# Optimization experiments

Hardware: AMD Instinct MI355X
Metric: run time of the kernel (lower is better)

The kernel has to match this reference:

```python
import jax, jax.numpy as jnp
import numpy as np

C_MID = 32  # inChannels // 8
# Packing order matches torch loop: diagonal offset -i for i in 0..C-1,
# i.e. pairs (j+i, j) for j in 0..C-1-i, concatenated.
_ROWS = np.concatenate([np.arange(C_MID - i) + i for i in range(C_MID)])
_COLS = np.concatenate([np.arange(C_MID - i) for i in range(C_MID)])


def _bn_relu(y, g, b, m, v, eps=1e-5):
    # y: (B, C, H, W); per-channel affine BN (eval-style) + relu
    inv = g / jnp.sqrt(v + eps)
    return jax.nn.relu(y * inv[:, None, None] + (b - m * inv)[:, None, None])


def setup_inputs() -> dict:
    key = jax.random.key(0)
    ks = jax.random.split(key, 14)
    B, Cin, H, W = 16, 256, 64, 64
    mid, T, Cout = C_MID, C_MID * (C_MID + 1) // 2, 256
    return {
        "x": jax.random.normal(ks[0], (B, Cin, H, W), jnp.float32),
        "w1": jax.random.normal(ks[1], (mid, Cin), jnp.float32) * 0.05,
        "b1": jax.random.normal(ks[2], (mid,), jnp.float32) * 0.05,
        "g1": jax.random.uniform(ks[3], (mid,), jnp.float32, 0.5, 1.5),
        "be1": jax.random.normal(ks[4], (mid,), jnp.float32) * 0.1,
        "m1": jax.random.normal(ks[5], (mid,), jnp.float32) * 0.1,
        "v1": jax.random.uniform(ks[6], (mid,), jnp.float32, 0.5, 1.5),
        "w2": jax.random.normal(ks[7], (Cout, T), jnp.float32) * 0.05,
        "b2": jax.random.normal(ks[8], (Cout,), jnp.float32) * 0.05,
        "g2": jax.random.uniform(ks[9], (Cout,), jnp.float32, 0.5, 1.5),
        "be2": jax.random.normal(ks[10], (Cout,), jnp.float32) * 0.1,
        "m2": jax.random.normal(ks[11], (Cout,), jnp.float32) * 0.1,
        "v2": jax.random.uniform(ks[12], (Cout,), jnp.float32, 0.5, 1.5),
    }


def reference(x, w1, b1, g1, be1, m1, v1, w2, b2, g2, be2, m2, v2):
    # dimReduceLayer1: 1x1 conv + BN + relu
    y = jnp.einsum('bchw,oc->bohw', x, w1) + b1[:, None, None]
    y = _bn_relu(y, g1, be1, m1, v1)                       # (B, mid, H, W)
    yb = jnp.transpose(y, (0, 2, 3, 1))                    # (B, H, W, mid)
    rows = jnp.asarray(_ROWS)
    cols = jnp.asarray(_COLS)
    # Packed lower-triangular bilinear features, exactly the torch diagonal+cat order.
    packed = yb[..., rows] * yb[..., cols]                 # (B, H, W, T)
    # dimReduceLayer2: 1x1 conv + BN + relu
    z = jnp.einsum('bhwt,ot->bohw', packed, w2) + b2[:, None, None]
    return _bn_relu(z, g2, be2, m2, v2)
```

## Files before the change

### kernel.cpp

```cpp
#include <hip/hip_runtime.h>

#define EPS 1e-5f

typedef float f32x4 __attribute__((ext_vector_type(4)));
typedef short bf16x8 __attribute__((ext_vector_type(8)));

__device__ __forceinline__ unsigned short f2bf(float f) {
  unsigned int u = __builtin_bit_cast(unsigned int, f);
  u = (u + 0x7FFFu + ((u >> 16) & 1u)) >> 16;
  return (unsigned short)u;
}

__global__ __launch_bounds__(256) void k_prep(
    const float* __restrict__ w1, const float* __restrict__ b1,
    const float* __restrict__ g1, const float* __restrict__ be1,
    const float* __restrict__ m1, const float* __restrict__ v1,
    const float* __restrict__ w2, const float* __restrict__ b2,
    const float* __restrict__ g2, const float* __restrict__ be2,
    const float* __restrict__ m2, const float* __restrict__ v2,
    float* __restrict__ beta1, float* __restrict__ beta2,
    unsigned short* __restrict__ w1b, unsigned short* __restrict__ w2f)
{
  int t = blockIdx.x * 256 + threadIdx.x;
  if (t < 139264) {
    int j = t & 7, l = (t >> 3) & 63, g = t >> 9;
    int ct = g & 15, ks = g >> 4;
    int k = ks * 32 + (l >> 4) * 8 + j;
    int ch = ct * 16 + (l & 15);
    float val = 0.f;
    if (k < 528) {
      float s2 = g2[ch] * rsqrtf(v2[ch] + EPS);
      val = w2[ch * 528 + k] * s2;
    }
    w2f[t] = f2bf(val);
  }
  if (t < 8192) {
    int j = t & 7, l = (t >> 3) & 63, g = t >> 9;
    int ct = g & 1, ks = g >> 1;
    int c = ks * 32 + (l >> 4) * 8 + j;
    int m = ct * 16 + (l & 15);
    float s1 = g1[m] * rsqrtf(v1[m] + EPS);
    w1b[t] = f2bf(w1[m * 256 + c] * s1);
  }
  if (t < 32) {
    float s1 = g1[t] * rsqrtf(v1[t] + EPS);
    beta1[t] = (b1[t] - m1[t]) * s1 + be1[t];
  }
  if (t < 256) {
    float s2 = g2[t] * rsqrtf(v2[t] + EPS);
    beta2[t] = (b2[t] - m2[t]) * s2 + be2[t];
  }
}

__global__ __launch_bounds__(256) void k_fused(
    const float* __restrict__ x, const unsigned short* __restrict__ w1b,
    const float* __restrict__ beta1, const unsigned short* __restrict__ w2f,
    const float* __restrict__ beta2, float* __restrict__ out)
{
  __shared__ __align__(16) unsigned short pk[64 * 548];
  __shared__ float yf[64 * 33];
  int tid = threadIdx.x;
  int wv = tid >> 6, lane = tid & 63;
  int l15 = lane & 15, l4 = lane >> 4;
  int pb = blockIdx.x * 64;
  int b = pb >> 12, hw0 = pb & 4095;
  const float* xb = x + ((size_t)b << 20) + hw0;

  unsigned short* xt = pk;
  {
    int q = tid & 15;
    int c40 = tid >> 4;
    for (int pass = 0; pass < 4; ++pass) {
      int c4 = c40 + pass * 16;
      float4 v[4];
#pragma unroll
      for (int i = 0; i < 4; ++i)
        v[i] = *(const float4*)&xb[(size_t)(4 * c4 + i) * 4096 + 4 * q];
#pragma unroll
      for (int s = 0; s < 4; ++s) {
        float e0 = ((const float*)&v[0])[s];
        float e1 = ((const float*)&v[1])[s];
        float e2 = ((const float*)&v[2])[s];
        float e3 = ((const float*)&v[3])[s];
        unsigned int lo = (unsigned int)f2bf(e0) | ((unsigned int)f2bf(e1) << 16);
        unsigned int hi = (unsigned int)f2bf(e2) | ((unsigned int)f2bf(e3) << 16);
        *(uint2*)&xt[(4 * q + s) * 276 + 4 * c4] = make_uint2(lo, hi);
      }
    }
  }
  __syncthreads();

  {
    f32x4 acc1[2];
    acc1[0] = (f32x4){0.f, 0.f, 0.f, 0.f};
    acc1[1] = (f32x4){0.f, 0.f, 0.f, 0.f};
    const uint4* w1b4 = (const uint4*)w1b;
    int px = wv * 16 + l15;
    for (int ks = 0; ks < 8; ++ks) {
      union { uint4 q; bf16x8 v; } A0, A1, B;
      A0.q = w1b4[(ks * 2 + 0) * 64 + lane];
      A1.q = w1b4[(ks * 2 + 1) * 64 + lane];
      const unsigned short* s = &xt[px * 276 + ks * 32 + l4 * 8];
      uint2 lo = *(const uint2*)s;
      uint2 hi = *(const uint2*)(s + 4);
      B.q = make_uint4(lo.x, lo.y, hi.x, hi.y);
      acc1[0] = __builtin_amdgcn_mfma_f32_16x16x32_bf16(A0.v, B.v, acc1[0], 0, 0, 0);
      acc1[1] = __builtin_amdgcn_mfma_f32_16x16x32_bf16(A1.v, B.v, acc1[1], 0, 0, 0);
    }
    __syncthreads();
#pragma unroll
    for (int ct = 0; ct < 2; ++ct) {
      int m0 = ct * 16 + l4 * 4;
#pragma unroll
      for (int r = 0; r < 4; ++r) {
        float yv = fmaxf(acc1[ct][r] + beta1[m0 + r], 0.f);
        yf[px * 33 + m0 + r] = yv;
      }
    }
  }
  __syncthreads();

  {
    int p2 = tid & 63, set = tid >> 6;
    const float* yr = &yf[p2 * 33];
    unsigned short* pr = &pk[p2 * 548];
    for (int i = set; i < 32; i += 4) {
      int base = 32 * i - (i * (i - 1)) / 2;
      int len = 32 - i;
      int j = 0;
      if (base & 1) {
        pr[base] = f2bf(yr[i] * yr[0]);
        j = 1;
      }
      for (; j + 1 < len; j += 2) {
        float a = yr[i + j] * yr[j];
        float c = yr[i + j + 1] * yr[j + 1];
        *(unsigned int*)&pr[base + j] =
            (unsigned int)f2bf(a) | ((unsigned int)f2bf(c) << 16);
      }
      if (j < len) pr[base + j] = f2bf(yr[i + j] * yr[j]);
    }
    if (tid < 64) {
      unsigned int* pru = (unsigned int*)pk + tid * 274;
#pragma unroll
      for (int z = 264; z < 274; ++z) pru[z] = 0u;
    }
  }
  __syncthreads();

  f32x4 acc[4][4];
#pragma unroll
  for (int a = 0; a < 4; ++a)
#pragma unroll
    for (int c = 0; c < 4; ++c)
      acc[a][c] = (f32x4){0.f, 0.f, 0.f, 0.f};

  const uint4* w2f4 = (const uint4*)w2f;
  for (int ks = 0; ks < 17; ++ks) {
    union { uint4 q; bf16x8 v; } A[4], B[4];
#pragma unroll
    for (int ctl = 0; ctl < 4; ++ctl)
      A[ctl].q = w2f4[(ks * 16 + wv * 4 + ctl) * 64 + lane];
#pragma unroll
    for (int pt = 0; pt < 4; ++pt) {
      const unsigned short* src = &pk[(pt * 16 + l15) * 548 + ks * 32 + l4 * 8];
      uint2 lo = *(const uint2*)src;
      uint2 hi = *(const uint2*)(src + 4);
      B[pt].q = make_uint4(lo.x, lo.y, hi.x, hi.y);
    }
#pragma unroll
    for (int pt = 0; pt < 4; ++pt)
#pragma unroll
      for (int ctl = 0; ctl < 4; ++ctl)
        acc[pt][ctl] = __builtin_amdgcn_mfma_f32_16x16x32_bf16(
            A[ctl].v, B[pt].v, acc[pt][ctl], 0, 0, 0);
  }

  float bet[4][4];
#pragma unroll
  for (int ctl = 0; ctl < 4; ++ctl)
#pragma unroll
    for (int r = 0; r < 4; ++r)
      bet[ctl][r] = beta2[(wv * 4 + ctl) * 16 + l4 * 4 + r];

#pragma unroll
  for (int pt = 0; pt < 4; ++pt) {
    int hw = hw0 + pt * 16 + l15;
#pragma unroll
    for (int ctl = 0; ctl < 4; ++ctl) {
      int ch = (wv * 4 + ctl) * 16 + l4 * 4;
#pragma unroll
      for (int r = 0; r < 4; ++r) {
        float v = fmaxf(acc[pt][ctl][r] + bet[ctl][r], 0.f);
        out[(((size_t)b * 256 + (ch + r)) << 12) + hw] = v;
      }
    }
  }
}

extern "C" void kernel_launch(void* const* d_in, const int* in_sizes, int n_in,
                              void* d_out, int out_size, void* d_ws, size_t ws_size,
                              hipStream_t stream)
{
  const float* x   = (const float*)d_in[0];
  const float* w1  = (const float*)d_in[1];
  const float* b1  = (const float*)d_in[2];
  const float* g1  = (const float*)d_in[3];
  const float* be1 = (const float*)d_in[4];
  const float* m1  = (const float*)d_in[5];
  const float* v1  = (const float*)d_in[6];
  const float* w2  = (const float*)d_in[7];
  const float* b2  = (const float*)d_in[8];
  const float* g2  = (const float*)d_in[9];
  const float* be2 = (const float*)d_in[10];
  const float* m2  = (const float*)d_in[11];
  const float* v2  = (const float*)d_in[12];

  char* ws = (char*)d_ws;
  float*          beta1 = (float*)(ws);
  float*          beta2 = (float*)(ws + 128);
  unsigned short* w1b   = (unsigned short*)(ws + 1152);
  unsigned short* w2f   = (unsigned short*)(ws + 17536);
  float* out = (float*)d_out;

  k_prep<<<dim3(544), dim3(256), 0, stream>>>(
      w1, b1, g1, be1, m1, v1, w2, b2, g2, be2, m2, v2, beta1, beta2, w1b, w2f);
  k_fused<<<dim3(1024), dim3(256), 0, stream>>>(x, w1b, beta1, w2f, beta2, out);
}
```

Before: 57.63 us.

## Halve pixel tile per block and unroll packed bilinear product generation

Each block now handles 32 pixels instead of 64, which halves LDS use and doubles the grid so more blocks fit per CU (launch bounds ask for 4). The first GEMM splits work across waves by pixel tile and channel tile, which also drops an extra barrier. The bilinear packing is rewritten with compile-time diagonals held in registers and balanced across 8 thread groups, replacing the strided runtime loop. In exchange, each block reloads the full w2 weight matrix for half as many pixels, so weight traffic per output doubles.

After: 48.62 us. -15.6%, faster.

```diff
diff --git a/kernel.cpp b/kernel.cpp
--- a/kernel.cpp
+++ b/kernel.cpp
@@ -52,26 +52,55 @@
   }
 }
 
-__global__ __launch_bounds__(256) void k_fused(
+template<int I>
+__device__ __forceinline__ void do_diag(const float* __restrict__ y,
+                                        unsigned short* __restrict__ pr)
+{
+  constexpr int L = 32 - I;
+  constexpr int base = 32 * I - (I * (I - 1)) / 2;
+  float p[L];
+#pragma unroll
+  for (int j = 0; j < L; ++j) p[j] = y[I + j] * y[j];
+  constexpr int s = (base & 1) ? 1 : 0;
+  if constexpr (s != 0) pr[base] = f2bf(p[0]);
+#pragma unroll
+  for (int j = s; j + 1 < L; j += 2)
+    *(unsigned int*)&pr[base + j] =
+        (unsigned int)f2bf(p[j]) | ((unsigned int)f2bf(p[j + 1]) << 16);
+  if constexpr (((L - s) & 1) != 0) pr[base + L - 1] = f2bf(p[L - 1]);
+}
+
+template<int S>
+__device__ __forceinline__ void do_set(const float* __restrict__ y,
+                                       unsigned short* __restrict__ pr)
+{
+  do_diag<S>(y, pr);
+  do_diag<31 - S>(y, pr);
+  do_diag<S + 8>(y, pr);
+  do_diag<23 - S>(y, pr);
+}
+
+__global__ __launch_bounds__(256, 4) void k_fused(
     const float* __restrict__ x, const unsigned short* __restrict__ w1b,
     const float* __restrict__ beta1, const unsigned short* __restrict__ w2f,
     const float* __restrict__ beta2, float* __restrict__ out)
 {
-  __shared__ __align__(16) unsigned short pk[64 * 548];
-  __shared__ float yf[64 * 33];
+  __shared__ __align__(16) unsigned short pk[32 * 548];
+  __shared__ __align__(8) float yf[32 * 34];
   int tid = threadIdx.x;
   int wv = tid >> 6, lane = tid & 63;
   int l15 = lane & 15, l4 = lane >> 4;
-  int pb = blockIdx.x * 64;
+  int pb = blockIdx.x * 32;
   int b = pb >> 12, hw0 = pb & 4095;
   const float* xb = x + ((size_t)b << 20) + hw0;
 
   unsigned short* xt = pk;
   {
-    int q = tid & 15;
-    int c40 = tid >> 4;
-    for (int pass = 0; pass < 4; ++pass) {
-      int c4 = c40 + pass * 16;
+    int q = tid & 7;
+    int cg = tid >> 3;
+#pragma unroll
+    for (int pass = 0; pass < 2; ++pass) {
+      int c4 = cg + pass * 32;
       float4 v[4];
 #pragma unroll
       for (int i = 0; i < 4; ++i)
@@ -91,85 +120,75 @@
   __syncthreads();
 
   {
-    f32x4 acc1[2];
-    acc1[0] = (f32x4){0.f, 0.f, 0.f, 0.f};
-    acc1[1] = (f32x4){0.f, 0.f, 0.f, 0.f};
+    int pxt = wv & 1, mt = wv >> 1;
+    int px = pxt * 16 + l15;
+    f32x4 acc1 = (f32x4){0.f, 0.f, 0.f, 0.f};
     const uint4* w1b4 = (const uint4*)w1b;
-    int px = wv * 16 + l15;
     for (int ks = 0; ks < 8; ++ks) {
-      union { uint4 q; bf16x8 v; } A0, A1, B;
-      A0.q = w1b4[(ks * 2 + 0) * 64 + lane];
-      A1.q = w1b4[(ks * 2 + 1) * 64 + lane];
+      union { uint4 q; bf16x8 v; } A, B;
+      A.q = w1b4[(ks * 2 + mt) * 64 + lane];
       const unsigned short* s = &xt[px * 276 + ks * 32 + l4 * 8];
       uint2 lo = *(const uint2*)s;
       uint2 hi = *(const uint2*)(s + 4);
       B.q = make_uint4(lo.x, lo.y, hi.x, hi.y);
-      acc1[0] = __builtin_amdgcn_mfma_f32_16x16x32_bf16(A0.v, B.v, acc1[0], 0, 0, 0);
-      acc1[1] = __builtin_amdgcn_mfma_f32_16x16x32_bf16(A1.v, B.v, acc1[1], 0, 0, 0);
-    }
-    __syncthreads();
-#pragma unroll
-    for (int ct = 0; ct < 2; ++ct) {
-      int m0 = ct * 16 + l4 * 4;
-#pragma unroll
-      for (int r = 0; r < 4; ++r) {
-        float yv = fmaxf(acc1[ct][r] + beta1[m0 + r], 0.f);
-        yf[px * 33 + m0 + r] = yv;
-      }
-    }
+      acc1 = __builtin_amdgcn_mfma_f32_16x16x32_bf16(A.v, B.v, acc1, 0, 0, 0);
+    }
+    int m0 = mt * 16 + l4 * 4;
+#pragma unroll
+    for (int r = 0; r < 4; ++r)
+      yf[px * 34 + m0 + r] = fmaxf(acc1[r] + beta1[m0 + r], 0.f);
   }
   __syncthreads();
 
   {
-    int p2 = tid & 63, set = tid >> 6;
-    const float* yr = &yf[p2 * 33];
-    unsigned short* pr = &pk[p2 * 548];
-    for (int i = set; i < 32; i += 4) {
-      int base = 32 * i - (i * (i - 1)) / 2;
-      int len = 32 - i;
-      int j = 0;
-      if (base & 1) {
-        pr[base] = f2bf(yr[i] * yr[0]);
-        j = 1;
-      }
-      for (; j + 1 < len; j += 2) {
-        float a = yr[i + j] * yr[j];
-        float c = yr[i + j + 1] * yr[j + 1];
-        *(unsigned int*)&pr[base + j] =
-            (unsigned int)f2bf(a) | ((unsigned int)f2bf(c) << 16);
-      }
-      if (j < len) pr[base + j] = f2bf(yr[i + j] * yr[j]);
-    }
-    if (tid < 64) {
-      unsigned int* pru = (unsigned int*)pk + tid * 274;
-#pragma unroll
-      for (int z = 264; z < 274; ++z) pru[z] = 0u;
+    int px2 = tid & 31, set = tid >> 5;
+    const float* yr = &yf[px2 * 34];
+    unsigned short* pr = &pk[px2 * 548];
+    float y[32];
+#pragma unroll
+    for (int k = 0; k < 16; ++k) {
+      float2 v = *(const float2*)&yr[2 * k];
+      y[2 * k] = v.x; y[2 * k + 1] = v.y;
+    }
+    switch (set) {
+      case 0: do_set<0>(y, pr); break;
+      case 1: do_set<1>(y, pr); break;
+      case 2: do_set<2>(y, pr); break;
+      case 3: do_set<3>(y, pr); break;
+      case 4: do_set<4>(y, pr); break;
+      case 5: do_set<5>(y, pr); break;
+      case 6: do_set<6>(y, pr); break;
+      default: do_set<7>(y, pr); break;
+    }
+    if (set < 4) {
+      *(unsigned int*)&pr[528 + set * 4] = 0u;
+      *(unsigned int*)&pr[530 + set * 4] = 0u;
     }
   }
   __syncthreads();
 
-  f32x4 acc[4][4];
-#pragma unroll
-  for (int a = 0; a < 4; ++a)
+  f32x4 acc[2][4];
+#pragma unroll
+  for (int a = 0; a < 2; ++a)
 #pragma unroll
     for (int c = 0; c < 4; ++c)
       acc[a][c] = (f32x4){0.f, 0.f, 0.f, 0.f};
 
   const uint4* w2f4 = (const uint4*)w2f;
   for (int ks = 0; ks < 17; ++ks) {
-    union { uint4 q; bf16x8 v; } A[4], B[4];
+    union { uint4 q; bf16x8 v; } A[4], B[2];
 #pragma unroll
     for (int ctl = 0; ctl < 4; ++ctl)
       A[ctl].q = w2f4[(ks * 16 + wv * 4 + ctl) * 64 + lane];
 #pragma unroll
-    for (int pt = 0; pt < 4; ++pt) {
+    for (int pt = 0; pt < 2; ++pt) {
       const unsigned short* src = &pk[(pt * 16 + l15) * 548 + ks * 32 + l4 * 8];
       uint2 lo = *(const uint2*)src;
       uint2 hi = *(const uint2*)(src + 4);
       B[pt].q = make_uint4(lo.x, lo.y, hi.x, hi.y);
     }
 #pragma unroll
-    for (int pt = 0; pt < 4; ++pt)
+    for (int pt = 0; pt < 2; ++pt)
 #pragma unroll
       for (int ctl = 0; ctl < 4; ++ctl)
         acc[pt][ctl] = __builtin_amdgcn_mfma_f32_16x16x32_bf16(
@@ -184,7 +203,7 @@
       bet[ctl][r] = beta2[(wv * 4 + ctl) * 16 + l4 * 4 + r];
 
 #pragma unroll
-  for (int pt = 0; pt < 4; ++pt) {
+  for (int pt = 0; pt < 2; ++pt) {
     int hw = hw0 + pt * 16 + l15;
 #pragma unroll
     for (int ctl = 0; ctl < 4; ++ctl) {
@@ -225,5 +244,5 @@
 
   k_prep<<<dim3(544), dim3(256), 0, stream>>>(
       w1, b1, g1, be1, m1, v1, w2, b2, g2, be2, m2, v2, beta1, beta2, w1b, w2f);
-  k_fused<<<dim3(1024), dim3(256), 0, stream>>>(x, w1b, beta1, w2f, beta2, out);
-}
+  k_fused<<<dim3(2048), dim3(256), 0, stream>>>(x, w1b, beta1, w2f, beta2, out);
+}
```
